# Kernel tuning notes

Measured on AMD Instinct MI355X. Metric: run time of the kernel, lower is better.

## Reference

```python
import jax, jax.numpy as jnp
import numpy as np

N, DMAX, IN, HID, OUT = 30000, 16, 128, 256, 64


def setup_inputs() -> dict:
    key = jax.random.key(0)
    ks = jax.random.split(key, 12)
    p = lambda k, shape: jax.random.normal(k, shape, dtype=jnp.float32) * 0.05
    return {
        "feat": jax.random.normal(ks[0], (N, IN), dtype=jnp.float32),
        "nbr_idx": jax.random.randint(ks[1], (N, DMAX), 0, N, dtype=jnp.int32),
        "deg": jax.random.randint(ks[2], (N,), 1, DMAX + 1, dtype=jnp.int32),
        # layer 1: LSTM(in=IN, hidden=IN), fc_self/fc_neigh: IN -> HID
        "Wih1": p(ks[3], (4 * IN, IN)),
        "Whh1": p(ks[4], (4 * IN, IN)),
        "bih1": jnp.zeros((4 * IN,), jnp.float32),
        "bhh1": jnp.zeros((4 * IN,), jnp.float32),
        "Wself1": p(ks[5], (HID, IN)),
        "Wneigh1": p(ks[6], (HID, IN)),
        "b1": jnp.zeros((HID,), jnp.float32),
        # layer 2: LSTM(in=HID, hidden=HID), fc_self/fc_neigh: HID -> OUT
        "Wih2": p(ks[7], (4 * HID, HID)),
        "Whh2": p(ks[8], (4 * HID, HID)),
        "bih2": jnp.zeros((4 * HID,), jnp.float32),
        "bhh2": jnp.zeros((4 * HID,), jnp.float32),
        "Wself2": p(ks[9], (OUT, HID)),
        "Wneigh2": p(ks[10], (OUT, HID)),
        "b2": jnp.zeros((OUT,), jnp.float32),
    }


def _lstm_agg(nbr_feats, deg, Wih, Whh, bih, bhh):
    """LSTM over padded neighbor sequences [N, D, F]; returns final hidden [N, H].
    Matches torch nn.LSTM gate order (i, f, g, o), zero initial state; padded
    steps (t >= deg) leave the state untouched, so result equals the hidden
    state at each node's true sequence length."""
    D = nbr_feats.shape[1]
    H = Whh.shape[1]
    h0 = jnp.zeros((nbr_feats.shape[0], H), nbr_feats.dtype)
    xs = (jnp.swapaxes(nbr_feats, 0, 1), jnp.arange(D))  # ([D,N,F], [D])

    def step(carry, x_t):
        h, c = carry
        x, t = x_t
        gates = x @ Wih.T + bih + h @ Whh.T + bhh  # [N, 4H]
        i, f, g, o = jnp.split(gates, 4, axis=-1)
        c_new = jax.nn.sigmoid(f) * c + jax.nn.sigmoid(i) * jnp.tanh(g)
        h_new = jax.nn.sigmoid(o) * jnp.tanh(c_new)
        valid = (t < deg)[:, None]
        return (jnp.where(valid, h_new, h), jnp.where(valid, c_new, c)), None

    (h, _), _ = jax.lax.scan(step, (h0, h0), xs)
    return h


def _sage_layer(x, nbr_idx, deg, Wih, Whh, bih, bhh, Wself, Wneigh, b):
    nbr = x[nbr_idx]  # gather: [N, DMAX, F]
    m = _lstm_agg(nbr, deg, Wih, Whh, bih, bhh)  # [N, H] (H == F)
    return x @ Wself.T + m @ Wneigh.T + b


def reference(feat, nbr_idx, deg,
              Wih1, Whh1, bih1, bhh1, Wself1, Wneigh1, b1,
              Wih2, Whh2, bih2, bhh2, Wself2, Wneigh2, b2):
    h = jax.nn.relu(_sage_layer(feat, nbr_idx, deg,
                                Wih1, Whh1, bih1, bhh1, Wself1, Wneigh1, b1))
    return _sage_layer(h, nbr_idx, deg,
                       Wih2, Whh2, bih2, bhh2, Wself2, Wneigh2, b2)
```

## Files before the change

### kernel.cpp

```cpp
#include <hip/hip_runtime.h>
#include <hip/hip_bf16.h>
#include <stdint.h>


#define NN 30000
#define DMAXX 16

typedef __bf16 bf16_t;
typedef __bf16 bf16x8 __attribute__((ext_vector_type(8)));
typedef float f32x4 __attribute__((ext_vector_type(4)));
typedef unsigned short u16x4 __attribute__((ext_vector_type(4)));

__device__ __align__(16) bf16_t g_hbuf[(size_t)NN * 256];
__device__ __align__(16) bf16_t g_xg1[(size_t)NN * 512];
__device__ __align__(16) bf16_t g_xg2[(size_t)NN * 1024];
__device__ __align__(16) bf16_t g_wbuf[753664];
__device__ int g_perm[NN];

#define OFF_WIH1 0
#define OFF_WHH1 65536
#define OFF_WSELF1 131072
#define OFF_WNEIGH1 163840
#define OFF_WIH2 196608
#define OFF_WHH2 458752
#define OFF_WSELF2 720896
#define OFF_WNEIGH2 737280
#define W_TOTAL 753664

__global__ __launch_bounds__(256)
void cvt_weights(const float* __restrict__ s0, const float* __restrict__ s1,
                 const float* __restrict__ s2, const float* __restrict__ s3,
                 const float* __restrict__ s4, const float* __restrict__ s5,
                 const float* __restrict__ s6, const float* __restrict__ s7)
{
    int i = (blockIdx.x * 256 + threadIdx.x) * 4;
    if (i >= W_TOTAL) return;
    const float* src; int off;
    if      (i < OFF_WHH1)   { src = s0; off = OFF_WIH1; }
    else if (i < OFF_WSELF1) { src = s1; off = OFF_WHH1; }
    else if (i < OFF_WNEIGH1){ src = s2; off = OFF_WSELF1; }
    else if (i < OFF_WIH2)   { src = s3; off = OFF_WNEIGH1; }
    else if (i < OFF_WHH2)   { src = s4; off = OFF_WIH2; }
    else if (i < OFF_WSELF2) { src = s5; off = OFF_WHH2; }
    else if (i < OFF_WNEIGH2){ src = s6; off = OFF_WSELF2; }
    else                     { src = s7; off = OFF_WNEIGH2; }
    float4 v = *reinterpret_cast<const float4*>(src + (i - off));
    bf16_t o[4] __attribute__((aligned(8)));
    o[0] = (bf16_t)v.x; o[1] = (bf16_t)v.y; o[2] = (bf16_t)v.z; o[3] = (bf16_t)v.w;
    *reinterpret_cast<uint2*>(&g_wbuf[i]) = *reinterpret_cast<const uint2*>(o);
}

__global__ __launch_bounds__(256)
void build_perm(const int* __restrict__ deg, int* __restrict__ perm)
{
    __shared__ int s_base[DMAXX + 1];
    const int tid = threadIdx.x;
    if (tid <= DMAXX) s_base[tid] = 0;
    __syncthreads();
    for (int i = tid; i < NN; i += 256) {
        int d = deg[i]; d = d < 0 ? 0 : (d > DMAXX ? DMAXX : d);
        atomicAdd(&s_base[d], 1);
    }
    __syncthreads();
    if (tid == 0) {
        int acc = 0;
        for (int d = DMAXX; d >= 0; --d) { int c = s_base[d]; s_base[d] = acc; acc += c; }
    }
    __syncthreads();
    for (int i = tid; i < NN; i += 256) {
        int d = deg[i]; d = d < 0 ? 0 : (d > DMAXX ? DMAXX : d);
        int p = atomicAdd(&s_base[d], 1);
        perm[p] = i;
    }
}

__device__ __forceinline__ float fsig(float x) { return 1.0f / (1.0f + __expf(-x)); }
__device__ __forceinline__ float ftanh(float x) { return 1.0f - 2.0f / (__expf(2.0f * x) + 1.0f); }
__device__ __forceinline__ float bf2f(unsigned short s) {
    union { unsigned u; float f; } v; v.u = ((unsigned)s) << 16; return v.f;
}

template<int F, int LDA, int NT, bool XF32>
__device__ __forceinline__ void stage_tile(bf16_t* dst, const void* src, int row0, int tid)
{
    constexpr int UN = F / 8;
    for (int e = tid; e < 64 * UN; e += NT) {
        int m = e / UN, sub = e - m * UN;
        int row = row0 + m; if (row >= NN) row = NN - 1;
        if constexpr (XF32) {
            const float* p = (const float*)src + (size_t)row * F + sub * 8;
            float4 f0 = reinterpret_cast<const float4*>(p)[0];
            float4 f1 = reinterpret_cast<const float4*>(p)[1];
            bf16_t t[8] __attribute__((aligned(16)));
            t[0]=(bf16_t)f0.x; t[1]=(bf16_t)f0.y; t[2]=(bf16_t)f0.z; t[3]=(bf16_t)f0.w;
            t[4]=(bf16_t)f1.x; t[5]=(bf16_t)f1.y; t[6]=(bf16_t)f1.z; t[7]=(bf16_t)f1.w;
            *reinterpret_cast<uint4*>(&dst[m * LDA + sub * 8]) = *reinterpret_cast<const uint4*>(t);
        } else {
            const bf16_t* p = (const bf16_t*)src + (size_t)row * F + sub * 8;
            *reinterpret_cast<uint4*>(&dst[m * LDA + sub * 8]) = *reinterpret_cast<const uint4*>(p);
        }
    }
}

template<int F, int LDA, int NT, bool XF32>
__device__ __forceinline__ void stage_rows(bf16_t* dst, const void* src, const int* nodes, int tid)
{
    constexpr int UN = F / 8;
    for (int e = tid; e < 64 * UN; e += NT) {
        int m = e / UN, sub = e - m * UN;
        int row = nodes[m];
        if constexpr (XF32) {
            const float* p = (const float*)src + (size_t)row * F + sub * 8;
            float4 f0 = reinterpret_cast<const float4*>(p)[0];
            float4 f1 = reinterpret_cast<const float4*>(p)[1];
            bf16_t t[8] __attribute__((aligned(16)));
            t[0]=(bf16_t)f0.x; t[1]=(bf16_t)f0.y; t[2]=(bf16_t)f0.z; t[3]=(bf16_t)f0.w;
            t[4]=(bf16_t)f1.x; t[5]=(bf16_t)f1.y; t[6]=(bf16_t)f1.z; t[7]=(bf16_t)f1.w;
            *reinterpret_cast<uint4*>(&dst[m * LDA + sub * 8]) = *reinterpret_cast<const uint4*>(t);
        } else {
            const bf16_t* p = (const bf16_t*)src + (size_t)row * F + sub * 8;
            *reinterpret_cast<uint4*>(&dst[m * LDA + sub * 8]) = *reinterpret_cast<const uint4*>(p);
        }
    }
}

template<int F, int G, int NW, bool XF32>
__global__ __launch_bounds__(NW * 64, 2)
void xg_gemm(const void* __restrict__ xsrc_v, const bf16_t* __restrict__ W,
             const float* __restrict__ b0, const float* __restrict__ b1v,
             bf16_t* __restrict__ xg)
{
    constexpr int LDA = F + 8, KK = F / 32, NT = NW * 64;
    constexpr int CPW = G / NW;
    constexpr int CT = CPW / 16;
    static_assert(CPW % 16 == 0 && F % 16 == 0, "");
    const int tid = threadIdx.x, wave = tid >> 6, lane = tid & 63;
    const int q = lane >> 4, m16 = lane & 15;
    const int row0 = blockIdx.x * 64;

    __shared__ __align__(16) bf16_t s_x[64 * LDA];
    stage_tile<F, LDA, NT, XF32>(s_x, xsrc_v, row0, tid);
    __syncthreads();

    #pragma unroll
    for (int ct = 0; ct < CT; ++ct) {
        const int lc0 = wave * CPW + ct * 16;
        const int g = lc0 / F, c0 = lc0 - g * F;
        const float bias = b0[lc0 + m16] + b1v[lc0 + m16];
        f32x4 acc[4];
        #pragma unroll
        for (int rt = 0; rt < 4; ++rt)
            #pragma unroll
            for (int r = 0; r < 4; ++r) acc[rt][r] = bias;
        #pragma unroll
        for (int kk = 0; kk < KK; ++kk) {
            const int ko = kk * 32 + q * 8;
            bf16x8 b = *reinterpret_cast<const bf16x8*>(W + (size_t)(lc0 + m16) * F + ko);
            #pragma unroll
            for (int rt = 0; rt < 4; ++rt) {
                bf16x8 a = *reinterpret_cast<const bf16x8*>(&s_x[(rt * 16 + m16) * LDA + ko]);
                acc[rt] = __builtin_amdgcn_mfma_f32_16x16x32_bf16(a, b, acc[rt], 0, 0, 0);
            }
        }
        #pragma unroll
        for (int rt = 0; rt < 4; ++rt)
            #pragma unroll
            for (int r = 0; r < 4; ++r) {
                int row = row0 + rt * 16 + q * 4 + r;
                if (row < NN)
                    xg[(size_t)row * G + (size_t)(c0 + m16) * 4 + g] = (bf16_t)acc[rt][r];
            }
    }
}

template<int F, int OUTF, bool RELU, bool XF32, typename OutT>
__global__ __launch_bounds__(1024, 4)
void sage_rec(const void* __restrict__ xself_v,
              const bf16_t* __restrict__ xg,
              const int* __restrict__ nbr_idx, const int* __restrict__ deg,
              const int* __restrict__ perm,
              const bf16_t* __restrict__ Whh,
              const bf16_t* __restrict__ Wself, const bf16_t* __restrict__ Wneigh,
              const float* __restrict__ bout, OutT* __restrict__ outp)
{
    constexpr int M = 64, LDA = F + 8, KK = F / 32, NW = 16, NT = 1024;
    constexpr int NWC = F / 16;
    constexpr int NWR = NW / NWC;
    constexpr int RT = M / (16 * NWR);
    constexpr int NPASS = RT / 2;
    constexpr int G4 = 4 * F;
    static_assert(NWC * NWR == NW && RT % 2 == 0, "");
    const int tid = threadIdx.x, wave = tid >> 6, lane = tid & 63;
    const int q = lane >> 4, m16 = lane & 15;
    const int wc = wave % NWC, wr = wave / NWC;
    const int ROWB = wr * (RT * 16);
    const int col = wc * 16 + m16;
    const int slot0 = blockIdx.x * M;

    __shared__ __align__(16) bf16_t s_h[2][M * LDA];
    __shared__ int s_idx[M * DMAXX];
    __shared__ int s_deg[M];
    __shared__ int s_node[M];
    __shared__ int s_tmax;

    for (int i = tid; i < M; i += NT) {
        int slot = slot0 + i; if (slot >= NN) slot = NN - 1;
        int node = perm[slot];
        s_node[i] = node;
        s_deg[i] = deg[node];
    }
    __syncthreads();
    for (int i = tid; i < M * DMAXX; i += NT) {
        int node = s_node[i >> 4];
        int v = nbr_idx[node * DMAXX + (i & 15)];
        if (v < 0) v = 0; if (v >= NN) v = NN - 1;
        s_idx[i] = v;
    }
    for (int i = tid; i < M * LDA; i += NT) s_h[0][i] = (bf16_t)0.0f;
    if (tid == 0) {
        int mx = 1;
        for (int i = 0; i < M; ++i) { int d = s_deg[i]; mx = d > mx ? d : mx; }
        s_tmax = mx;
    }
    __syncthreads();
    const int tmax = s_tmax;

    f32x4 c0, c1, c2, c3;
    #pragma unroll
    for (int r = 0; r < 4; ++r) { c0[r]=0.f; c1[r]=0.f; c2[r]=0.f; c3[r]=0.f; }

    auto do_pass = [&](int rtb, f32x4& cA, f32x4& cB,
                       const bf16_t* cur, bf16_t* nxt, int t) {
        u16x4 u[2][4];
        #pragma unroll
        for (int j = 0; j < 2; ++j)
            #pragma unroll
            for (int r = 0; r < 4; ++r) {
                int row = s_idx[(ROWB + (rtb + j) * 16 + q * 4 + r) * DMAXX + t];
                u[j][r] = *reinterpret_cast<const u16x4*>(
                    xg + (size_t)row * G4 + (size_t)col * 4);
            }
        f32x4 acc[2][4];
        #pragma unroll
        for (int j = 0; j < 2; ++j)
            #pragma unroll
            for (int g = 0; g < 4; ++g)
                #pragma unroll
                for (int r = 0; r < 4; ++r) acc[j][g][r] = 0.0f;
        #pragma unroll
        for (int kk = 0; kk < KK; ++kk) {
            const int ko = kk * 32 + q * 8;
            bf16x8 ah0 = *reinterpret_cast<const bf16x8*>(
                &cur[(ROWB + rtb * 16 + m16) * LDA + ko]);
            bf16x8 ah1 = *reinterpret_cast<const bf16x8*>(
                &cur[(ROWB + (rtb + 1) * 16 + m16) * LDA + ko]);
            #pragma unroll
            for (int g = 0; g < 4; ++g) {
                bf16x8 bh = *reinterpret_cast<const bf16x8*>(
                    Whh + (size_t)(g * F + col) * F + ko);
                acc[0][g] = __builtin_amdgcn_mfma_f32_16x16x32_bf16(ah0, bh, acc[0][g], 0, 0, 0);
                acc[1][g] = __builtin_amdgcn_mfma_f32_16x16x32_bf16(ah1, bh, acc[1][g], 0, 0, 0);
            }
        }
        #pragma unroll
        for (int j = 0; j < 2; ++j) {
            f32x4& cc = j ? cB : cA;
            #pragma unroll
            for (int r = 0; r < 4; ++r) {
                int rowr = ROWB + (rtb + j) * 16 + q * 4 + r;
                float iv = fsig (acc[j][0][r] + bf2f(u[j][r].x));
                float fv = fsig (acc[j][1][r] + bf2f(u[j][r].y));
                float gv = ftanh(acc[j][2][r] + bf2f(u[j][r].z));
                float ov = fsig (acc[j][3][r] + bf2f(u[j][r].w));
                float cn = fv * cc[r] + iv * gv;
                float hv = ov * ftanh(cn);
                const int pos = rowr * LDA + col;
                int d = s_deg[rowr];
                if (t < d) {
                    cc[r] = cn;
                    nxt[pos] = (bf16_t)hv;
                } else if (t == d) {
                    reinterpret_cast<unsigned short*>(nxt)[pos] =
                        reinterpret_cast<const unsigned short*>(cur)[pos];
                }
            }
        }
    };

    #pragma unroll 1
    for (int t = 0; t < tmax; ++t) {
        const bf16_t* cur = s_h[t & 1];
        bf16_t* nxt = s_h[(t + 1) & 1];
        do_pass(0, c0, c1, cur, nxt, t);
        if constexpr (NPASS > 1) {
            __builtin_amdgcn_sched_barrier(0);
            do_pass(2, c2, c3, cur, nxt, t);
        }
        __syncthreads();
    }

    const int fb = tmax & 1;
    const bf16_t* hfin = s_h[fb];
    bf16_t* hstage = s_h[fb ^ 1];
    stage_rows<F, LDA, NT, XF32>(hstage, xself_v, s_node, tid);
    __syncthreads();

    constexpr int NCT = OUTF / 16;
    constexpr int TILES = NCT * 4;
    constexpr int TPW = TILES / NW;
    static_assert(TILES % NW == 0, "");
    #pragma unroll
    for (int tt = 0; tt < TPW; ++tt) {
        int tile = wave * TPW + tt;
        int ot = tile % NCT, rt = tile / NCT;
        f32x4 o;
        o[0] = 0.f; o[1] = 0.f; o[2] = 0.f; o[3] = 0.f;
        #pragma unroll
        for (int kk = 0; kk < KK; ++kk) {
            const int ko = kk * 32 + q * 8;
            bf16x8 axs = *reinterpret_cast<const bf16x8*>(&hstage[(rt * 16 + m16) * LDA + ko]);
            bf16x8 am  = *reinterpret_cast<const bf16x8*>(&hfin[(rt * 16 + m16) * LDA + ko]);
            bf16x8 bs = *reinterpret_cast<const bf16x8*>(Wself  + (size_t)(ot * 16 + m16) * F + ko);
            bf16x8 bn = *reinterpret_cast<const bf16x8*>(Wneigh + (size_t)(ot * 16 + m16) * F + ko);
            o = __builtin_amdgcn_mfma_f32_16x16x32_bf16(axs, bs, o, 0, 0, 0);
            o = __builtin_amdgcn_mfma_f32_16x16x32_bf16(am,  bn, o, 0, 0, 0);
        }
        int ocol = ot * 16 + m16;
        float bias = bout[ocol];
        #pragma unroll
        for (int r = 0; r < 4; ++r) {
            int node = s_node[rt * 16 + q * 4 + r];
            float v = o[r] + bias;
            if (RELU) v = fmaxf(v, 0.0f);
            outp[(size_t)node * OUTF + ocol] = (OutT)v;
        }
    }
}

extern "C" void kernel_launch(void* const* d_in, const int* in_sizes, int n_in,
                              void* d_out, int out_size, void* d_ws, size_t ws_size,
                              hipStream_t stream)
{
    const float* feat    = (const float*)d_in[0];
    const int*   nbr     = (const int*)d_in[1];
    const int*   degp    = (const int*)d_in[2];
    const float* Wih1    = (const float*)d_in[3];
    const float* Whh1    = (const float*)d_in[4];
    const float* bih1    = (const float*)d_in[5];
    const float* bhh1    = (const float*)d_in[6];
    const float* Wself1  = (const float*)d_in[7];
    const float* Wneigh1 = (const float*)d_in[8];
    const float* b1      = (const float*)d_in[9];
    const float* Wih2    = (const float*)d_in[10];
    const float* Whh2    = (const float*)d_in[11];
    const float* bih2    = (const float*)d_in[12];
    const float* bhh2    = (const float*)d_in[13];
    const float* Wself2  = (const float*)d_in[14];
    const float* Wneigh2 = (const float*)d_in[15];
    const float* b2      = (const float*)d_in[16];

    bf16_t *hglob, *wglob, *xg1, *xg2;
    int *permg;
    hipGetSymbolAddress((void**)&hglob, HIP_SYMBOL(g_hbuf));
    hipGetSymbolAddress((void**)&wglob, HIP_SYMBOL(g_wbuf));
    hipGetSymbolAddress((void**)&xg1,   HIP_SYMBOL(g_xg1));
    hipGetSymbolAddress((void**)&xg2,   HIP_SYMBOL(g_xg2));
    hipGetSymbolAddress((void**)&permg, HIP_SYMBOL(g_perm));

    cvt_weights<<<W_TOTAL / 4 / 256, 256, 0, stream>>>(
        Wih1, Whh1, Wself1, Wneigh1, Wih2, Whh2, Wself2, Wneigh2);

    build_perm<<<1, 256, 0, stream>>>(degp, permg);

    const int grid = (NN + 63) / 64;

    xg_gemm<128, 512, 8, true><<<grid, 512, 0, stream>>>(
        feat, wglob + OFF_WIH1, bih1, bhh1, xg1);

    sage_rec<128, 256, true, true, bf16_t><<<grid, 1024, 0, stream>>>(
        feat, xg1, nbr, degp, permg, wglob + OFF_WHH1,
        wglob + OFF_WSELF1, wglob + OFF_WNEIGH1, b1, hglob);

    xg_gemm<256, 1024, 8, false><<<grid, 512, 0, stream>>>(
        hglob, wglob + OFF_WIH2, bih2, bhh2, xg2);

    sage_rec<256, 64, false, false, float><<<grid, 1024, 0, stream>>>(
        hglob, xg2, nbr, degp, permg, wglob + OFF_WHH2,
        wglob + OFF_WSELF2, wglob + OFF_WNEIGH2, b2, (float*)d_out);
}
```

Before: 1.026 ms.

## Fuse LSTM input projection into recurrent kernel and prefetch neighbor features

Removes the separate input-gate GEMM kernels and their large per-node gate buffers. The recurrent kernel instead gathers raw neighbor feature rows into shared memory each step and multiplies them by Wih alongside the Whh product. The next step's neighbor rows are prefetched into registers to overlap the gather with compute. This cuts gather bytes per neighbor by four times but recomputes the input projection per neighbor visit, roughly doubling MFMA work in the recurrence and adding shared memory and syncs.

Result: slower. 2.131 ms (+107.8%).

```diff
diff --git a/kernel.cpp b/kernel.cpp
--- a/kernel.cpp
+++ b/kernel.cpp
@@ -9,11 +9,9 @@
 typedef __bf16 bf16_t;
 typedef __bf16 bf16x8 __attribute__((ext_vector_type(8)));
 typedef float f32x4 __attribute__((ext_vector_type(4)));
-typedef unsigned short u16x4 __attribute__((ext_vector_type(4)));
 
 __device__ __align__(16) bf16_t g_hbuf[(size_t)NN * 256];
-__device__ __align__(16) bf16_t g_xg1[(size_t)NN * 512];
-__device__ __align__(16) bf16_t g_xg2[(size_t)NN * 1024];
+__device__ __align__(16) bf16_t g_fbuf[(size_t)NN * 128];
 __device__ __align__(16) bf16_t g_wbuf[753664];
 __device__ int g_perm[NN];
 
@@ -51,6 +49,18 @@
 }
 
 __global__ __launch_bounds__(256)
+void cvt_feat(const float* __restrict__ src, bf16_t* __restrict__ dst)
+{
+    int i = (blockIdx.x * 256 + threadIdx.x) * 8;
+    float4 f0 = *reinterpret_cast<const float4*>(src + i);
+    float4 f1 = *reinterpret_cast<const float4*>(src + i + 4);
+    bf16_t t[8] __attribute__((aligned(16)));
+    t[0]=(bf16_t)f0.x; t[1]=(bf16_t)f0.y; t[2]=(bf16_t)f0.z; t[3]=(bf16_t)f0.w;
+    t[4]=(bf16_t)f1.x; t[5]=(bf16_t)f1.y; t[6]=(bf16_t)f1.z; t[7]=(bf16_t)f1.w;
+    *reinterpret_cast<uint4*>(&dst[i]) = *reinterpret_cast<const uint4*>(t);
+}
+
+__global__ __launch_bounds__(256)
 void build_perm(const int* __restrict__ deg, int* __restrict__ perm)
 {
     __shared__ int s_base[DMAXX + 1];
@@ -76,110 +86,27 @@
 
 __device__ __forceinline__ float fsig(float x) { return 1.0f / (1.0f + __expf(-x)); }
 __device__ __forceinline__ float ftanh(float x) { return 1.0f - 2.0f / (__expf(2.0f * x) + 1.0f); }
-__device__ __forceinline__ float bf2f(unsigned short s) {
-    union { unsigned u; float f; } v; v.u = ((unsigned)s) << 16; return v.f;
-}
-
-template<int F, int LDA, int NT, bool XF32>
-__device__ __forceinline__ void stage_tile(bf16_t* dst, const void* src, int row0, int tid)
-{
-    constexpr int UN = F / 8;
-    for (int e = tid; e < 64 * UN; e += NT) {
-        int m = e / UN, sub = e - m * UN;
-        int row = row0 + m; if (row >= NN) row = NN - 1;
-        if constexpr (XF32) {
-            const float* p = (const float*)src + (size_t)row * F + sub * 8;
-            float4 f0 = reinterpret_cast<const float4*>(p)[0];
-            float4 f1 = reinterpret_cast<const float4*>(p)[1];
-            bf16_t t[8] __attribute__((aligned(16)));
-            t[0]=(bf16_t)f0.x; t[1]=(bf16_t)f0.y; t[2]=(bf16_t)f0.z; t[3]=(bf16_t)f0.w;
-            t[4]=(bf16_t)f1.x; t[5]=(bf16_t)f1.y; t[6]=(bf16_t)f1.z; t[7]=(bf16_t)f1.w;
-            *reinterpret_cast<uint4*>(&dst[m * LDA + sub * 8]) = *reinterpret_cast<const uint4*>(t);
-        } else {
-            const bf16_t* p = (const bf16_t*)src + (size_t)row * F + sub * 8;
-            *reinterpret_cast<uint4*>(&dst[m * LDA + sub * 8]) = *reinterpret_cast<const uint4*>(p);
-        }
-    }
-}
-
-template<int F, int LDA, int NT, bool XF32>
-__device__ __forceinline__ void stage_rows(bf16_t* dst, const void* src, const int* nodes, int tid)
+
+template<int F, int LDA, int NT>
+__device__ __forceinline__ void stage_rows(bf16_t* dst, const bf16_t* src, const int* nodes, int tid)
 {
     constexpr int UN = F / 8;
     for (int e = tid; e < 64 * UN; e += NT) {
         int m = e / UN, sub = e - m * UN;
         int row = nodes[m];
-        if constexpr (XF32) {
-            const float* p = (const float*)src + (size_t)row * F + sub * 8;
-            float4 f0 = reinterpret_cast<const float4*>(p)[0];
-            float4 f1 = reinterpret_cast<const float4*>(p)[1];
-            bf16_t t[8] __attribute__((aligned(16)));
-            t[0]=(bf16_t)f0.x; t[1]=(bf16_t)f0.y; t[2]=(bf16_t)f0.z; t[3]=(bf16_t)f0.w;
-            t[4]=(bf16_t)f1.x; t[5]=(bf16_t)f1.y; t[6]=(bf16_t)f1.z; t[7]=(bf16_t)f1.w;
-            *reinterpret_cast<uint4*>(&dst[m * LDA + sub * 8]) = *reinterpret_cast<const uint4*>(t);
-        } else {
-            const bf16_t* p = (const bf16_t*)src + (size_t)row * F + sub * 8;
-            *reinterpret_cast<uint4*>(&dst[m * LDA + sub * 8]) = *reinterpret_cast<const uint4*>(p);
-        }
-    }
-}
-
-template<int F, int G, int NW, bool XF32>
-__global__ __launch_bounds__(NW * 64, 2)
-void xg_gemm(const void* __restrict__ xsrc_v, const bf16_t* __restrict__ W,
-             const float* __restrict__ b0, const float* __restrict__ b1v,
-             bf16_t* __restrict__ xg)
-{
-    constexpr int LDA = F + 8, KK = F / 32, NT = NW * 64;
-    constexpr int CPW = G / NW;
-    constexpr int CT = CPW / 16;
-    static_assert(CPW % 16 == 0 && F % 16 == 0, "");
-    const int tid = threadIdx.x, wave = tid >> 6, lane = tid & 63;
-    const int q = lane >> 4, m16 = lane & 15;
-    const int row0 = blockIdx.x * 64;
-
-    __shared__ __align__(16) bf16_t s_x[64 * LDA];
-    stage_tile<F, LDA, NT, XF32>(s_x, xsrc_v, row0, tid);
-    __syncthreads();
-
-    #pragma unroll
-    for (int ct = 0; ct < CT; ++ct) {
-        const int lc0 = wave * CPW + ct * 16;
-        const int g = lc0 / F, c0 = lc0 - g * F;
-        const float bias = b0[lc0 + m16] + b1v[lc0 + m16];
-        f32x4 acc[4];
-        #pragma unroll
-        for (int rt = 0; rt < 4; ++rt)
-            #pragma unroll
-            for (int r = 0; r < 4; ++r) acc[rt][r] = bias;
-        #pragma unroll
-        for (int kk = 0; kk < KK; ++kk) {
-            const int ko = kk * 32 + q * 8;
-            bf16x8 b = *reinterpret_cast<const bf16x8*>(W + (size_t)(lc0 + m16) * F + ko);
-            #pragma unroll
-            for (int rt = 0; rt < 4; ++rt) {
-                bf16x8 a = *reinterpret_cast<const bf16x8*>(&s_x[(rt * 16 + m16) * LDA + ko]);
-                acc[rt] = __builtin_amdgcn_mfma_f32_16x16x32_bf16(a, b, acc[rt], 0, 0, 0);
-            }
-        }
-        #pragma unroll
-        for (int rt = 0; rt < 4; ++rt)
-            #pragma unroll
-            for (int r = 0; r < 4; ++r) {
-                int row = row0 + rt * 16 + q * 4 + r;
-                if (row < NN)
-                    xg[(size_t)row * G + (size_t)(c0 + m16) * 4 + g] = (bf16_t)acc[rt][r];
-            }
-    }
-}
-
-template<int F, int OUTF, bool RELU, bool XF32, typename OutT>
+        const bf16_t* p = src + (size_t)row * F + sub * 8;
+        *reinterpret_cast<uint4*>(&dst[m * LDA + sub * 8]) = *reinterpret_cast<const uint4*>(p);
+    }
+}
+
+template<int F, int OUTF, bool RELU, typename OutT>
 __global__ __launch_bounds__(1024, 4)
-void sage_rec(const void* __restrict__ xself_v,
-              const bf16_t* __restrict__ xg,
+void sage_rec(const bf16_t* __restrict__ xself,
+              const bf16_t* __restrict__ xnbr,
               const int* __restrict__ nbr_idx, const int* __restrict__ deg,
               const int* __restrict__ perm,
-              const bf16_t* __restrict__ Whh,
+              const bf16_t* __restrict__ Wih, const bf16_t* __restrict__ Whh,
+              const float* __restrict__ bih, const float* __restrict__ bhh,
               const bf16_t* __restrict__ Wself, const bf16_t* __restrict__ Wneigh,
               const float* __restrict__ bout, OutT* __restrict__ outp)
 {
@@ -188,8 +115,9 @@
     constexpr int NWR = NW / NWC;
     constexpr int RT = M / (16 * NWR);
     constexpr int NPASS = RT / 2;
-    constexpr int G4 = 4 * F;
-    static_assert(NWC * NWR == NW && RT % 2 == 0, "");
+    constexpr int UNX = F / 8;
+    constexpr int NPF = (M * UNX) / NT;
+    static_assert(NWC * NWR == NW && RT % 2 == 0 && (M * UNX) % NT == 0, "");
     const int tid = threadIdx.x, wave = tid >> 6, lane = tid & 63;
     const int q = lane >> 4, m16 = lane & 15;
     const int wc = wave % NWC, wr = wave / NWC;
@@ -198,6 +126,7 @@
     const int slot0 = blockIdx.x * M;
 
     __shared__ __align__(16) bf16_t s_h[2][M * LDA];
+    __shared__ __align__(16) bf16_t s_x[M * LDA];
     __shared__ int s_idx[M * DMAXX];
     __shared__ int s_deg[M];
     __shared__ int s_node[M];
@@ -225,39 +154,60 @@
     __syncthreads();
     const int tmax = s_tmax;
 
+    float bias4[4];
+    #pragma unroll
+    for (int g = 0; g < 4; ++g) bias4[g] = bih[g * F + col] + bhh[g * F + col];
+
+    auto ld_nbr = [&](int t, uint4* pf) {
+        #pragma unroll
+        for (int i = 0; i < NPF; ++i) {
+            int e = tid + i * NT;
+            int m = e / UNX, sub = e - m * UNX;
+            int row = s_idx[m * DMAXX + t];
+            pf[i] = *reinterpret_cast<const uint4*>(xnbr + (size_t)row * F + sub * 8);
+        }
+    };
+    auto st_nbr = [&](const uint4* pf) {
+        #pragma unroll
+        for (int i = 0; i < NPF; ++i) {
+            int e = tid + i * NT;
+            int m = e / UNX, sub = e - m * UNX;
+            *reinterpret_cast<uint4*>(&s_x[m * LDA + sub * 8]) = pf[i];
+        }
+    };
+
     f32x4 c0, c1, c2, c3;
     #pragma unroll
     for (int r = 0; r < 4; ++r) { c0[r]=0.f; c1[r]=0.f; c2[r]=0.f; c3[r]=0.f; }
 
     auto do_pass = [&](int rtb, f32x4& cA, f32x4& cB,
                        const bf16_t* cur, bf16_t* nxt, int t) {
-        u16x4 u[2][4];
-        #pragma unroll
-        for (int j = 0; j < 2; ++j)
-            #pragma unroll
-            for (int r = 0; r < 4; ++r) {
-                int row = s_idx[(ROWB + (rtb + j) * 16 + q * 4 + r) * DMAXX + t];
-                u[j][r] = *reinterpret_cast<const u16x4*>(
-                    xg + (size_t)row * G4 + (size_t)col * 4);
-            }
         f32x4 acc[2][4];
         #pragma unroll
         for (int j = 0; j < 2; ++j)
             #pragma unroll
             for (int g = 0; g < 4; ++g)
                 #pragma unroll
-                for (int r = 0; r < 4; ++r) acc[j][g][r] = 0.0f;
+                for (int r = 0; r < 4; ++r) acc[j][g][r] = bias4[g];
         #pragma unroll
         for (int kk = 0; kk < KK; ++kk) {
             const int ko = kk * 32 + q * 8;
+            bf16x8 ax0 = *reinterpret_cast<const bf16x8*>(
+                &s_x[(ROWB + rtb * 16 + m16) * LDA + ko]);
+            bf16x8 ax1 = *reinterpret_cast<const bf16x8*>(
+                &s_x[(ROWB + (rtb + 1) * 16 + m16) * LDA + ko]);
             bf16x8 ah0 = *reinterpret_cast<const bf16x8*>(
                 &cur[(ROWB + rtb * 16 + m16) * LDA + ko]);
             bf16x8 ah1 = *reinterpret_cast<const bf16x8*>(
                 &cur[(ROWB + (rtb + 1) * 16 + m16) * LDA + ko]);
             #pragma unroll
             for (int g = 0; g < 4; ++g) {
+                bf16x8 bi = *reinterpret_cast<const bf16x8*>(
+                    Wih + (size_t)(g * F + col) * F + ko);
                 bf16x8 bh = *reinterpret_cast<const bf16x8*>(
                     Whh + (size_t)(g * F + col) * F + ko);
+                acc[0][g] = __builtin_amdgcn_mfma_f32_16x16x32_bf16(ax0, bi, acc[0][g], 0, 0, 0);
+                acc[1][g] = __builtin_amdgcn_mfma_f32_16x16x32_bf16(ax1, bi, acc[1][g], 0, 0, 0);
                 acc[0][g] = __builtin_amdgcn_mfma_f32_16x16x32_bf16(ah0, bh, acc[0][g], 0, 0, 0);
                 acc[1][g] = __builtin_amdgcn_mfma_f32_16x16x32_bf16(ah1, bh, acc[1][g], 0, 0, 0);
             }
@@ -268,10 +218,10 @@
             #pragma unroll
             for (int r = 0; r < 4; ++r) {
                 int rowr = ROWB + (rtb + j) * 16 + q * 4 + r;
-                float iv = fsig (acc[j][0][r] + bf2f(u[j][r].x));
-                float fv = fsig (acc[j][1][r] + bf2f(u[j][r].y));
-                float gv = ftanh(acc[j][2][r] + bf2f(u[j][r].z));
-                float ov = fsig (acc[j][3][r] + bf2f(u[j][r].w));
+                float iv = fsig (acc[j][0][r]);
+                float fv = fsig (acc[j][1][r]);
+                float gv = ftanh(acc[j][2][r]);
+                float ov = fsig (acc[j][3][r]);
                 float cn = fv * cc[r] + iv * gv;
                 float hv = ov * ftanh(cn);
                 const int pos = rowr * LDA + col;
@@ -287,22 +237,36 @@
         }
     };
 
+    {
+        uint4 pf[NPF];
+        ld_nbr(0, pf);
+        st_nbr(pf);
+    }
+    __syncthreads();
+
     #pragma unroll 1
     for (int t = 0; t < tmax; ++t) {
         const bf16_t* cur = s_h[t & 1];
         bf16_t* nxt = s_h[(t + 1) & 1];
+        uint4 pf[NPF];
+        const bool havepf = (t + 1 < tmax);
+        if (havepf) ld_nbr(t + 1, pf);
         do_pass(0, c0, c1, cur, nxt, t);
         if constexpr (NPASS > 1) {
             __builtin_amdgcn_sched_barrier(0);
             do_pass(2, c2, c3, cur, nxt, t);
         }
         __syncthreads();
+        if (havepf) {
+            st_nbr(pf);
+            __syncthreads();
+        }
     }
 
     const int fb = tmax & 1;
     const bf16_t* hfin = s_h[fb];
     bf16_t* hstage = s_h[fb ^ 1];
-    stage_rows<F, LDA, NT, XF32>(hstage, xself_v, s_node, tid);
+    stage_rows<F, LDA, NT>(hstage, xself, s_node, tid);
     __syncthreads();
 
     constexpr int NCT = OUTF / 16;
@@ -359,32 +323,29 @@
     const float* Wneigh2 = (const float*)d_in[15];
     const float* b2      = (const float*)d_in[16];
 
-    bf16_t *hglob, *wglob, *xg1, *xg2;
+    bf16_t *hglob, *wglob, *fglob;
     int *permg;
     hipGetSymbolAddress((void**)&hglob, HIP_SYMBOL(g_hbuf));
     hipGetSymbolAddress((void**)&wglob, HIP_SYMBOL(g_wbuf));
-    hipGetSymbolAddress((void**)&xg1,   HIP_SYMBOL(g_xg1));
-    hipGetSymbolAddress((void**)&xg2,   HIP_SYMBOL(g_xg2));
+    hipGetSymbolAddress((void**)&fglob, HIP_SYMBOL(g_fbuf));
     hipGetSymbolAddress((void**)&permg, HIP_SYMBOL(g_perm));
 
     cvt_weights<<<W_TOTAL / 4 / 256, 256, 0, stream>>>(
         Wih1, Whh1, Wself1, Wneigh1, Wih2, Whh2, Wself2, Wneigh2);
 
+    cvt_feat<<<NN * 128 / 8 / 256, 256, 0, stream>>>(feat, fglob);
+
     build_perm<<<1, 256, 0, stream>>>(degp, permg);
 
     const int grid = (NN + 63) / 64;
 
-    xg_gemm<128, 512, 8, true><<<grid, 512, 0, stream>>>(
-        feat, wglob + OFF_WIH1, bih1, bhh1, xg1);
-
-    sage_rec<128, 256, true, true, bf16_t><<<grid, 1024, 0, stream>>>(
-        feat, xg1, nbr, degp, permg, wglob + OFF_WHH1,
+    sage_rec<128, 256, true, bf16_t><<<grid, 1024, 0, stream>>>(
+        fglob, fglob, nbr, degp, permg,
+        wglob + OFF_WIH1, wglob + OFF_WHH1, bih1, bhh1,
         wglob + OFF_WSELF1, wglob + OFF_WNEIGH1, b1, hglob);
 
-    xg_gemm<256, 1024, 8, false><<<grid, 512, 0, stream>>>(
-        hglob, wglob + OFF_WIH2, bih2, bhh2, xg2);
-
-    sage_rec<256, 64, false, false, float><<<grid, 1024, 0, stream>>>(
-        hglob, xg2, nbr, degp, permg, wglob + OFF_WHH2,
+    sage_rec<256, 64, false, float><<<grid, 1024, 0, stream>>>(
+        hglob, hglob, nbr, degp, permg,
+        wglob + OFF_WIH2, wglob + OFF_WHH2, bih2, bhh2,
         wglob + OFF_WSELF2, wglob + OFF_WNEIGH2, b2, (float*)d_out);
 }
```

## Halve recurrent kernel block to 8 waves, each covering all rows for its column slice

Applied to the files above, without the earlier changes.

The LSTM recurrence kernel drops from 1024 to 512 threads per block. Each wave now owns a contiguous column slice (16 or 32 columns) across all 64 rows instead of a 2D row/column tile, running two or four MFMA passes per timestep. This loads each Whh B fragment once per wave for more rows and makes the per-step barrier cheaper, at the cost of more serial work and registers per wave and less latency hiding from fewer waves per block. The epilogue tile mapping now also relies on NW=8.

New measurement: 1.602 ms. 56.2% more time.

```diff
diff --git a/kernel.cpp b/kernel.cpp
--- a/kernel.cpp
+++ b/kernel.cpp
@@ -174,7 +174,7 @@
 }
 
 template<int F, int OUTF, bool RELU, bool XF32, typename OutT>
-__global__ __launch_bounds__(1024, 4)
+__global__ __launch_bounds__(512, 4)
 void sage_rec(const void* __restrict__ xself_v,
               const bf16_t* __restrict__ xg,
               const int* __restrict__ nbr_idx, const int* __restrict__ deg,
@@ -183,18 +183,14 @@
               const bf16_t* __restrict__ Wself, const bf16_t* __restrict__ Wneigh,
               const float* __restrict__ bout, OutT* __restrict__ outp)
 {
-    constexpr int M = 64, LDA = F + 8, KK = F / 32, NW = 16, NT = 1024;
-    constexpr int NWC = F / 16;
-    constexpr int NWR = NW / NWC;
-    constexpr int RT = M / (16 * NWR);
-    constexpr int NPASS = RT / 2;
+    constexpr int M = 64, LDA = F + 8, KK = F / 32, NW = 8, NT = 512;
+    constexpr int CPW = F / NW;
+    constexpr int CT2 = CPW / 16;
     constexpr int G4 = 4 * F;
-    static_assert(NWC * NWR == NW && RT % 2 == 0, "");
+    static_assert(CT2 == 1 || CT2 == 2, "");
     const int tid = threadIdx.x, wave = tid >> 6, lane = tid & 63;
     const int q = lane >> 4, m16 = lane & 15;
-    const int wc = wave % NWC, wr = wave / NWC;
-    const int ROWB = wr * (RT * 16);
-    const int col = wc * 16 + m16;
+    const int colb = wave * CPW + m16;
     const int slot0 = blockIdx.x * M;
 
     __shared__ __align__(16) bf16_t s_h[2][M * LDA];
@@ -225,18 +221,21 @@
     __syncthreads();
     const int tmax = s_tmax;
 
-    f32x4 c0, c1, c2, c3;
+    f32x4 cA0, cA1, cA2, cA3, cB0, cB1, cB2, cB3;
     #pragma unroll
-    for (int r = 0; r < 4; ++r) { c0[r]=0.f; c1[r]=0.f; c2[r]=0.f; c3[r]=0.f; }
-
-    auto do_pass = [&](int rtb, f32x4& cA, f32x4& cB,
+    for (int r = 0; r < 4; ++r) {
+        cA0[r]=0.f; cA1[r]=0.f; cA2[r]=0.f; cA3[r]=0.f;
+        cB0[r]=0.f; cB1[r]=0.f; cB2[r]=0.f; cB3[r]=0.f;
+    }
+
+    auto do_pass = [&](int col, int rtb, f32x4& cX, f32x4& cY,
                        const bf16_t* cur, bf16_t* nxt, int t) {
         u16x4 u[2][4];
         #pragma unroll
         for (int j = 0; j < 2; ++j)
             #pragma unroll
             for (int r = 0; r < 4; ++r) {
-                int row = s_idx[(ROWB + (rtb + j) * 16 + q * 4 + r) * DMAXX + t];
+                int row = s_idx[((rtb + j) * 16 + q * 4 + r) * DMAXX + t];
                 u[j][r] = *reinterpret_cast<const u16x4*>(
                     xg + (size_t)row * G4 + (size_t)col * 4);
             }
@@ -251,9 +250,9 @@
         for (int kk = 0; kk < KK; ++kk) {
             const int ko = kk * 32 + q * 8;
             bf16x8 ah0 = *reinterpret_cast<const bf16x8*>(
-                &cur[(ROWB + rtb * 16 + m16) * LDA + ko]);
+                &cur[(rtb * 16 + m16) * LDA + ko]);
             bf16x8 ah1 = *reinterpret_cast<const bf16x8*>(
-                &cur[(ROWB + (rtb + 1) * 16 + m16) * LDA + ko]);
+                &cur[((rtb + 1) * 16 + m16) * LDA + ko]);
             #pragma unroll
             for (int g = 0; g < 4; ++g) {
                 bf16x8 bh = *reinterpret_cast<const bf16x8*>(
@@ -264,10 +263,10 @@
         }
         #pragma unroll
         for (int j = 0; j < 2; ++j) {
-            f32x4& cc = j ? cB : cA;
+            f32x4& cc = j ? cY : cX;
             #pragma unroll
             for (int r = 0; r < 4; ++r) {
-                int rowr = ROWB + (rtb + j) * 16 + q * 4 + r;
+                int rowr = (rtb + j) * 16 + q * 4 + r;
                 float iv = fsig (acc[j][0][r] + bf2f(u[j][r].x));
                 float fv = fsig (acc[j][1][r] + bf2f(u[j][r].y));
                 float gv = ftanh(acc[j][2][r] + bf2f(u[j][r].z));
@@ -291,10 +290,14 @@
     for (int t = 0; t < tmax; ++t) {
         const bf16_t* cur = s_h[t & 1];
         bf16_t* nxt = s_h[(t + 1) & 1];
-        do_pass(0, c0, c1, cur, nxt, t);
-        if constexpr (NPASS > 1) {
+        do_pass(colb, 0, cA0, cA1, cur, nxt, t);
+        __builtin_amdgcn_sched_barrier(0);
+        do_pass(colb, 2, cA2, cA3, cur, nxt, t);
+        if constexpr (CT2 > 1) {
             __builtin_amdgcn_sched_barrier(0);
-            do_pass(2, c2, c3, cur, nxt, t);
+            do_pass(colb + 16, 0, cB0, cB1, cur, nxt, t);
+            __builtin_amdgcn_sched_barrier(0);
+            do_pass(colb + 16, 2, cB2, cB3, cur, nxt, t);
         }
         __syncthreads();
     }
@@ -377,14 +380,14 @@
     xg_gemm<128, 512, 8, true><<<grid, 512, 0, stream>>>(
         feat, wglob + OFF_WIH1, bih1, bhh1, xg1);
 
-    sage_rec<128, 256, true, true, bf16_t><<<grid, 1024, 0, stream>>>(
+    sage_rec<128, 256, true, true, bf16_t><<<grid, 512, 0, stream>>>(
         feat, xg1, nbr, degp, permg, wglob + OFF_WHH1,
         wglob + OFF_WSELF1, wglob + OFF_WNEIGH1, b1, hglob);
 
     xg_gemm<256, 1024, 8, false><<<grid, 512, 0, stream>>>(
         hglob, wglob + OFF_WIH2, bih2, bhh2, xg2);
 
-    sage_rec<256, 64, false, false, float><<<grid, 1024, 0, stream>>>(
+    sage_rec<256, 64, false, false, float><<<grid, 512, 0, stream>>>(
         hglob, xg2, nbr, degp, permg, wglob + OFF_WHH2,
         wglob + OFF_WSELF2, wglob + OFF_WNEIGH2, b2, (float*)d_out);
 }
```

## Fuse layer-2 input-gate GEMM into layer-1 recurrent kernel epilogue

Applied to the files above, without the earlier changes.

The layer-1 sage_rec epilogue now keeps its output tile in shared memory and immediately multiplies it by Wih2, adding the biases, to write xg2 directly. This removes the separate xg_gemm launch and its re-read of the layer-1 hidden output from global memory. In exchange, the tail of each layer-1 block gets longer, register pressure may rise from holding the output accumulators, and the existing shared buffer is reused, which needs extra barriers.

After: 1.028 ms. About the same (+0.2%).

```diff
diff --git a/kernel.cpp b/kernel.cpp
--- a/kernel.cpp
+++ b/kernel.cpp
@@ -173,7 +173,7 @@
     }
 }
 
-template<int F, int OUTF, bool RELU, bool XF32, typename OutT>
+template<int F, int OUTF, bool RELU, bool XF32, typename OutT, bool FUSEXG>
 __global__ __launch_bounds__(1024, 4)
 void sage_rec(const void* __restrict__ xself_v,
               const bf16_t* __restrict__ xg,
@@ -181,7 +181,9 @@
               const int* __restrict__ perm,
               const bf16_t* __restrict__ Whh,
               const bf16_t* __restrict__ Wself, const bf16_t* __restrict__ Wneigh,
-              const float* __restrict__ bout, OutT* __restrict__ outp)
+              const float* __restrict__ bout, OutT* __restrict__ outp,
+              const bf16_t* __restrict__ Wih2, const float* __restrict__ bih2,
+              const float* __restrict__ bhh2, bf16_t* __restrict__ xg2out)
 {
     constexpr int M = 64, LDA = F + 8, KK = F / 32, NW = 16, NT = 1024;
     constexpr int NWC = F / 16;
@@ -309,30 +311,109 @@
     constexpr int TILES = NCT * 4;
     constexpr int TPW = TILES / NW;
     static_assert(TILES % NW == 0, "");
-    #pragma unroll
-    for (int tt = 0; tt < TPW; ++tt) {
-        int tile = wave * TPW + tt;
-        int ot = tile % NCT, rt = tile / NCT;
-        f32x4 o;
-        o[0] = 0.f; o[1] = 0.f; o[2] = 0.f; o[3] = 0.f;
-        #pragma unroll
-        for (int kk = 0; kk < KK; ++kk) {
-            const int ko = kk * 32 + q * 8;
-            bf16x8 axs = *reinterpret_cast<const bf16x8*>(&hstage[(rt * 16 + m16) * LDA + ko]);
-            bf16x8 am  = *reinterpret_cast<const bf16x8*>(&hfin[(rt * 16 + m16) * LDA + ko]);
-            bf16x8 bs = *reinterpret_cast<const bf16x8*>(Wself  + (size_t)(ot * 16 + m16) * F + ko);
-            bf16x8 bn = *reinterpret_cast<const bf16x8*>(Wneigh + (size_t)(ot * 16 + m16) * F + ko);
-            o = __builtin_amdgcn_mfma_f32_16x16x32_bf16(axs, bs, o, 0, 0, 0);
-            o = __builtin_amdgcn_mfma_f32_16x16x32_bf16(am,  bn, o, 0, 0, 0);
-        }
-        int ocol = ot * 16 + m16;
-        float bias = bout[ocol];
-        #pragma unroll
-        for (int r = 0; r < 4; ++r) {
-            int node = s_node[rt * 16 + q * 4 + r];
-            float v = o[r] + bias;
-            if (RELU) v = fmaxf(v, 0.0f);
-            outp[(size_t)node * OUTF + ocol] = (OutT)v;
+
+    if constexpr (!FUSEXG) {
+        #pragma unroll
+        for (int tt = 0; tt < TPW; ++tt) {
+            int tile = wave * TPW + tt;
+            int ot = tile % NCT, rt = tile / NCT;
+            f32x4 o;
+            o[0] = 0.f; o[1] = 0.f; o[2] = 0.f; o[3] = 0.f;
+            #pragma unroll
+            for (int kk = 0; kk < KK; ++kk) {
+                const int ko = kk * 32 + q * 8;
+                bf16x8 axs = *reinterpret_cast<const bf16x8*>(&hstage[(rt * 16 + m16) * LDA + ko]);
+                bf16x8 am  = *reinterpret_cast<const bf16x8*>(&hfin[(rt * 16 + m16) * LDA + ko]);
+                bf16x8 bs = *reinterpret_cast<const bf16x8*>(Wself  + (size_t)(ot * 16 + m16) * F + ko);
+                bf16x8 bn = *reinterpret_cast<const bf16x8*>(Wneigh + (size_t)(ot * 16 + m16) * F + ko);
+                o = __builtin_amdgcn_mfma_f32_16x16x32_bf16(axs, bs, o, 0, 0, 0);
+                o = __builtin_amdgcn_mfma_f32_16x16x32_bf16(am,  bn, o, 0, 0, 0);
+            }
+            int ocol = ot * 16 + m16;
+            float bias = bout[ocol];
+            #pragma unroll
+            for (int r = 0; r < 4; ++r) {
+                int node = s_node[rt * 16 + q * 4 + r];
+                float v = o[r] + bias;
+                if (RELU) v = fmaxf(v, 0.0f);
+                outp[(size_t)node * OUTF + ocol] = (OutT)v;
+            }
+        }
+    } else {
+        f32x4 ov[TPW];
+        #pragma unroll
+        for (int tt = 0; tt < TPW; ++tt) {
+            int tile = wave * TPW + tt;
+            int ot = tile % NCT, rt = tile / NCT;
+            f32x4 o;
+            o[0] = 0.f; o[1] = 0.f; o[2] = 0.f; o[3] = 0.f;
+            #pragma unroll
+            for (int kk = 0; kk < KK; ++kk) {
+                const int ko = kk * 32 + q * 8;
+                bf16x8 axs = *reinterpret_cast<const bf16x8*>(&hstage[(rt * 16 + m16) * LDA + ko]);
+                bf16x8 am  = *reinterpret_cast<const bf16x8*>(&hfin[(rt * 16 + m16) * LDA + ko]);
+                bf16x8 bs = *reinterpret_cast<const bf16x8*>(Wself  + (size_t)(ot * 16 + m16) * F + ko);
+                bf16x8 bn = *reinterpret_cast<const bf16x8*>(Wneigh + (size_t)(ot * 16 + m16) * F + ko);
+                o = __builtin_amdgcn_mfma_f32_16x16x32_bf16(axs, bs, o, 0, 0, 0);
+                o = __builtin_amdgcn_mfma_f32_16x16x32_bf16(am,  bn, o, 0, 0, 0);
+            }
+            ov[tt] = o;
+        }
+        __syncthreads();
+
+        constexpr int S1P = OUTF + 8;
+        static_assert(2 * M * LDA >= M * S1P, "s1 must fit in s_h");
+        bf16_t* s1 = &s_h[0][0];
+        #pragma unroll
+        for (int tt = 0; tt < TPW; ++tt) {
+            int tile = wave * TPW + tt;
+            int ot = tile % NCT, rt = tile / NCT;
+            int ocol = ot * 16 + m16;
+            float bias = bout[ocol];
+            #pragma unroll
+            for (int r = 0; r < 4; ++r) {
+                int rowi = rt * 16 + q * 4 + r;
+                int node = s_node[rowi];
+                float v = ov[tt][r] + bias;
+                if (RELU) v = fmaxf(v, 0.0f);
+                outp[(size_t)node * OUTF + ocol] = (OutT)v;
+                s1[rowi * S1P + ocol] = (bf16_t)v;
+            }
+        }
+        __syncthreads();
+
+        constexpr int G2 = 4 * OUTF;
+        constexpr int KK2 = OUTF / 32;
+        constexpr int CPW2 = G2 / NW;
+        constexpr int CT2 = CPW2 / 16;
+        #pragma unroll
+        for (int ct = 0; ct < CT2; ++ct) {
+            const int lc0 = wave * CPW2 + ct * 16;
+            const int g = lc0 / OUTF, cc0 = lc0 - g * OUTF;
+            const float bias2 = bih2[lc0 + m16] + bhh2[lc0 + m16];
+            f32x4 acc2[4];
+            #pragma unroll
+            for (int rt = 0; rt < 4; ++rt)
+                #pragma unroll
+                for (int r = 0; r < 4; ++r) acc2[rt][r] = bias2;
+            #pragma unroll
+            for (int kk = 0; kk < KK2; ++kk) {
+                const int ko = kk * 32 + q * 8;
+                bf16x8 b = *reinterpret_cast<const bf16x8*>(
+                    Wih2 + (size_t)(lc0 + m16) * OUTF + ko);
+                #pragma unroll
+                for (int rt = 0; rt < 4; ++rt) {
+                    bf16x8 a = *reinterpret_cast<const bf16x8*>(&s1[(rt * 16 + m16) * S1P + ko]);
+                    acc2[rt] = __builtin_amdgcn_mfma_f32_16x16x32_bf16(a, b, acc2[rt], 0, 0, 0);
+                }
+            }
+            #pragma unroll
+            for (int rt = 0; rt < 4; ++rt)
+                #pragma unroll
+                for (int r = 0; r < 4; ++r) {
+                    int node = s_node[rt * 16 + q * 4 + r];
+                    xg2out[(size_t)node * G2 + (size_t)(cc0 + m16) * 4 + g] = (bf16_t)acc2[rt][r];
+                }
         }
     }
 }
@@ -377,14 +458,13 @@
     xg_gemm<128, 512, 8, true><<<grid, 512, 0, stream>>>(
         feat, wglob + OFF_WIH1, bih1, bhh1, xg1);
 
-    sage_rec<128, 256, true, true, bf16_t><<<grid, 1024, 0, stream>>>(
+    sage_rec<128, 256, true, true, bf16_t, true><<<grid, 1024, 0, stream>>>(
         feat, xg1, nbr, degp, permg, wglob + OFF_WHH1,
-        wglob + OFF_WSELF1, wglob + OFF_WNEIGH1, b1, hglob);
-
-    xg_gemm<256, 1024, 8, false><<<grid, 512, 0, stream>>>(
-        hglob, wglob + OFF_WIH2, bih2, bhh2, xg2);
-
-    sage_rec<256, 64, false, false, float><<<grid, 1024, 0, stream>>>(
+        wglob + OFF_WSELF1, wglob + OFF_WNEIGH1, b1, hglob,
+        wglob + OFF_WIH2, bih2, bhh2, xg2);
+
+    sage_rec<256, 64, false, false, float, false><<<grid, 1024, 0, stream>>>(
         hglob, xg2, nbr, degp, permg, wglob + OFF_WHH2,
-        wglob + OFF_WSELF2, wglob + OFF_WNEIGH2, b2, (float*)d_out);
-}
+        wglob + OFF_WSELF2, wglob + OFF_WNEIGH2, b2, (float*)d_out,
+        nullptr, nullptr, nullptr, nullptr);
+}
```
